# Optimization experiments

Measured on AMD Instinct MI355X. Metric: run time of the kernel, lower is better.

The kernel has to match this reference:

```python
import jax, jax.numpy as jnp
import numpy as np

N = 100000
K = 27  # 3^3 kernel offsets for dimension=3
EPS = 1e-6


def layer_norm(x, gamma, beta):
    mu = jnp.mean(x, axis=-1, keepdims=True)
    var = jnp.mean(jnp.square(x - mu), axis=-1, keepdims=True)
    return (x - mu) * jax.lax.rsqrt(var + EPS) * gamma + beta


def sparse_conv3(x, idx, mask, W):
    # gather-GEMM-scatter form of Minkowski sparse conv:
    # x: [N, Cin], idx/mask: [N, K], W: [K, Cin, Cout]
    xg = jnp.where(mask[..., None], x[idx], 0.0)  # [N, K, Cin]
    return jnp.einsum('nkc,kcd->nd', xg, W)


def setup_inputs() -> dict:
    key = jax.random.key(0)
    ks = jax.random.split(key, 6)
    x = jax.random.normal(ks[0], (N, 32), dtype=jnp.float32)
    neighbor_idx = jax.random.randint(ks[1], (N, K), 0, N, dtype=jnp.int32)
    neighbor_mask = jax.random.randint(ks[2], (N, K), 0, 2) > 0
    W_conv = jax.random.normal(ks[3], (32, 32), dtype=jnp.float32) * 0.1
    W1 = jax.random.normal(ks[4], (K, 32, 128), dtype=jnp.float32) * 0.05
    W2 = jax.random.normal(ks[5], (K, 128, 32), dtype=jnp.float32) * 0.05
    return {
        'x': x,
        'neighbor_idx': neighbor_idx,
        'neighbor_mask': neighbor_mask,
        'W_conv': W_conv,
        'gamma0': jnp.ones((32,), jnp.float32),
        'beta0': jnp.zeros((32,), jnp.float32),
        'W1': W1,
        'gamma1': jnp.ones((128,), jnp.float32),
        'beta1': jnp.zeros((128,), jnp.float32),
        'W2': W2,
        'gamma2': jnp.ones((32,), jnp.float32),
        'beta2': jnp.zeros((32,), jnp.float32),
    }


def reference(x, neighbor_idx, neighbor_mask, W_conv, gamma0, beta0,
              W1, gamma1, beta1, W2, gamma2, beta2):
    gelu = lambda t: jax.nn.gelu(t, approximate=False)  # torch default (erf)
    residual = x
    out = x @ W_conv                      # kernel_size=1 conv == dense matmul
    out = gelu(layer_norm(out, gamma0, beta0))
    out = sparse_conv3(out, neighbor_idx, neighbor_mask, W1)
    out = gelu(layer_norm(out, gamma1, beta1))
    out = sparse_conv3(out, neighbor_idx, neighbor_mask, W2)
    out = layer_norm(out, gamma2, beta2)
    out = out + residual
    return gelu(out)
```

## Files before the change

### kernel.cpp

```cpp
#include <hip/hip_runtime.h>
#include <hip/hip_bf16.h>
#include <math.h>

#define NPTS 100000
#define KOFF 27

typedef __attribute__((ext_vector_type(8))) __bf16 bf16x8;
typedef __attribute__((ext_vector_type(4))) float f32x4;

__device__ __forceinline__ unsigned short f2bf(float f) {
    unsigned int u = __float_as_uint(f);
    u += 0x7fffu + ((u >> 16) & 1u);
    return (unsigned short)(u >> 16);
}

__device__ __forceinline__ float gelu_erf(float v) {
    return 0.5f * v * (1.0f + erff(v * 0.70710678118654752f));
}

__global__ __launch_bounds__(256)
void repack_kernel(const float* __restrict__ W1, const float* __restrict__ W2,
                   const void* __restrict__ maskp,
                   unsigned short* __restrict__ W1p,
                   unsigned short* __restrict__ W2p,
                   int* __restrict__ flagp) {
    int o = blockIdx.x * 256 + threadIdx.x;
    if (o == 0) {
        const unsigned int* mw = (const unsigned int*)maskp;
        int f = 0;
        for (int i = 0; i < 64; ++i) f |= (mw[i] > 1u) ? 1 : 0;
        *flagp = f;
    }
    if (o < KOFF * 32 * 128) {
        int j = o & 7, lane = (o >> 3) & 63;
        int quad = lane >> 4, nn = lane & 15;
        int ct1 = (o >> 9) & 7, k1 = o >> 12;
        int kk1 = quad * 8 + j;
        W1p[o] = f2bf(W1[(k1 * 32 + kk1) * 128 + (ct1 * 16 + nn)]);
        int ct2 = (o >> 9) & 1, kc2 = (o >> 10) & 3, k2 = o >> 12;
        int kk2 = kc2 * 32 + quad * 8 + j;
        W2p[o] = f2bf(W2[(k2 * 128 + kk2) * 32 + (ct2 * 16 + nn)]);
    }
}

__global__ __launch_bounds__(256)
void conv1_ln_gelu(const float* __restrict__ x, const float* __restrict__ Wc,
                   const float* __restrict__ g0, const float* __restrict__ b0,
                   unsigned short* __restrict__ out0) {
    __shared__ float xs[256];
    __shared__ float wc[1024];
    int t = threadIdx.x;
    int nb = blockIdx.x * 8;
    xs[t] = x[nb * 32 + t];
    for (int i = t; i < 1024; i += 256) wc[i] = Wc[i];
    __syncthreads();
    int r = t >> 5, d = t & 31;
    const float* xr = &xs[r * 32];
    float v = 0.f;
#pragma unroll
    for (int c = 0; c < 32; ++c) v = fmaf(xr[c], wc[c * 32 + d], v);
    float s = v, s2 = v * v;
#pragma unroll
    for (int m = 16; m >= 1; m >>= 1) {
        s  += __shfl_xor(s,  m, 32);
        s2 += __shfl_xor(s2, m, 32);
    }
    float mu  = s * (1.f / 32.f);
    float var = s2 * (1.f / 32.f) - mu * mu;
    float y = (v - mu) * rsqrtf(var + 1e-6f) * g0[d] + b0[d];
    out0[nb * 32 + t] = f2bf(gelu_erf(y));
}

__device__ __forceinline__ void stage_gidx64(int* s_gidx, const int* nidx,
                                             const void* maskp, int mflag,
                                             int nb, int t) {
    int cnt = (NPTS - nb < 64 ? NPTS - nb : 64) * KOFF;
    for (int i = t; i < 64 * KOFF; i += 64) {
        int g = -1;
        if (i < cnt) {
            int gi = nidx[nb * KOFF + i];
            int m = mflag ? (int)((const unsigned char*)maskp)[nb * KOFF + i]
                          : ((const int*)maskp)[nb * KOFF + i];
            g = m ? gi : -1;
        }
        s_gidx[i] = g;
    }
}

__global__ __launch_bounds__(64, 2)
void conv_k1(const int* __restrict__ nidx, const void* __restrict__ maskp,
             const int* __restrict__ flagp,
             const unsigned short* __restrict__ out0,
             const unsigned short* __restrict__ W1p,
             const float* __restrict__ g1, const float* __restrict__ b1,
             unsigned short* __restrict__ out1) {
    __shared__ int s_gidx[64 * KOFF];

    int t = threadIdx.x;
    int nb = blockIdx.x * 64;
    int mflag = *flagp;
    stage_gidx64(s_gidx, nidx, maskp, mflag, nb, t);
    __syncthreads();

    int lane = t & 63;
    int mrow = lane & 15, quad = lane >> 4;
    const unsigned short* a_base = out0 + quad * 8;
    const int* gp0 = &s_gidx[(0 * 16 + mrow) * KOFF];
    const int* gp1 = &s_gidx[(1 * 16 + mrow) * KOFF];
    const int* gp2 = &s_gidx[(2 * 16 + mrow) * KOFF];
    const int* gp3 = &s_gidx[(3 * 16 + mrow) * KOFF];

    f32x4 acc[4][8] = {};
    bf16x8 a[2][4], b[2][8];

    {
        const unsigned short* wb = W1p + (lane << 3);
#pragma unroll
        for (int ct = 0; ct < 8; ++ct)
            b[0][ct] = *reinterpret_cast<const bf16x8*>(wb + ((ct * 64) << 3));
        int g0 = gp0[0], g1i = gp1[0], g2 = gp2[0], g3 = gp3[0];
        a[0][0] = bf16x8{}; if (g0  >= 0) a[0][0] = *reinterpret_cast<const bf16x8*>(a_base + g0  * 32);
        a[0][1] = bf16x8{}; if (g1i >= 0) a[0][1] = *reinterpret_cast<const bf16x8*>(a_base + g1i * 32);
        a[0][2] = bf16x8{}; if (g2  >= 0) a[0][2] = *reinterpret_cast<const bf16x8*>(a_base + g2  * 32);
        a[0][3] = bf16x8{}; if (g3  >= 0) a[0][3] = *reinterpret_cast<const bf16x8*>(a_base + g3  * 32);
    }

#pragma unroll
    for (int k = 0; k < KOFF; ++k) {
        int cur = k & 1, nxt = cur ^ 1;
        if (k + 1 < KOFF) {
            const unsigned short* wb = W1p + ((((k + 1) * 8) * 64 + lane) << 3);
#pragma unroll
            for (int ct = 0; ct < 8; ++ct)
                b[nxt][ct] = *reinterpret_cast<const bf16x8*>(wb + ((ct * 64) << 3));
            int g0 = gp0[k + 1], g1i = gp1[k + 1], g2 = gp2[k + 1], g3 = gp3[k + 1];
            a[nxt][0] = bf16x8{}; if (g0  >= 0) a[nxt][0] = *reinterpret_cast<const bf16x8*>(a_base + g0  * 32);
            a[nxt][1] = bf16x8{}; if (g1i >= 0) a[nxt][1] = *reinterpret_cast<const bf16x8*>(a_base + g1i * 32);
            a[nxt][2] = bf16x8{}; if (g2  >= 0) a[nxt][2] = *reinterpret_cast<const bf16x8*>(a_base + g2  * 32);
            a[nxt][3] = bf16x8{}; if (g3  >= 0) a[nxt][3] = *reinterpret_cast<const bf16x8*>(a_base + g3  * 32);
        }
#pragma unroll
        for (int rt = 0; rt < 4; ++rt)
#pragma unroll
            for (int ct = 0; ct < 8; ++ct)
                acc[rt][ct] = __builtin_amdgcn_mfma_f32_16x16x32_bf16(a[cur][rt], b[cur][ct], acc[rt][ct], 0, 0, 0);
    }

    float gv[8], bv[8];
#pragma unroll
    for (int ct = 0; ct < 8; ++ct) {
        gv[ct] = g1[ct * 16 + mrow];
        bv[ct] = b1[ct * 16 + mrow];
    }
#pragma unroll
    for (int rt = 0; rt < 4; ++rt) {
        int n_base = nb + rt * 16 + quad * 4;
#pragma unroll
        for (int r = 0; r < 4; ++r) {
            float s = 0.f, s2 = 0.f;
#pragma unroll
            for (int ct = 0; ct < 8; ++ct) { float v = acc[rt][ct][r]; s += v; s2 += v * v; }
#pragma unroll
            for (int m = 1; m <= 8; m <<= 1) {
                s  += __shfl_xor(s,  m, 16);
                s2 += __shfl_xor(s2, m, 16);
            }
            float mu = s * (1.f / 128.f);
            float rs = rsqrtf(s2 * (1.f / 128.f) - mu * mu + 1e-6f);
            int n = n_base + r;
            if (n < NPTS) {
#pragma unroll
                for (int ct = 0; ct < 8; ++ct) {
                    float y = (acc[rt][ct][r] - mu) * rs * gv[ct] + bv[ct];
                    out1[n * 128 + ct * 16 + mrow] = f2bf(gelu_erf(y));
                }
            }
        }
    }
}

__global__ __launch_bounds__(64, 2)
void gemm_tmp(const unsigned short* __restrict__ out1,
              const unsigned short* __restrict__ W2p,
              unsigned short* __restrict__ tmp) {
    int t = threadIdx.x;
    int nb = blockIdx.x * 64;
    int mrow = t & 15, quad = t >> 4;

    bf16x8 a[4][4];
#pragma unroll
    for (int rt = 0; rt < 4; ++rt) {
        int n = nb + rt * 16 + mrow;
        bool ok = (n < NPTS);
#pragma unroll
        for (int kc = 0; kc < 4; ++kc) {
            a[rt][kc] = bf16x8{};
            if (ok)
                a[rt][kc] = *reinterpret_cast<const bf16x8*>(out1 + (size_t)n * 128 + kc * 32 + quad * 8);
        }
    }
    bf16x8 b[2][8];
    {
        const unsigned short* wb = W2p + (t << 3);
#pragma unroll
        for (int f = 0; f < 8; ++f)
            b[0][f] = *reinterpret_cast<const bf16x8*>(wb + ((f * 64) << 3));
    }

#pragma unroll
    for (int k = 0; k < KOFF; ++k) {
        int cur = k & 1, nxt = cur ^ 1;
        if (k + 1 < KOFF) {
            const unsigned short* wb = W2p + ((((k + 1) * 8) * 64 + t) << 3);
#pragma unroll
            for (int f = 0; f < 8; ++f)
                b[nxt][f] = *reinterpret_cast<const bf16x8*>(wb + ((f * 64) << 3));
        }
        f32x4 acc[4][2] = {};
#pragma unroll
        for (int rt = 0; rt < 4; ++rt)
#pragma unroll
            for (int kc = 0; kc < 4; ++kc) {
                acc[rt][0] = __builtin_amdgcn_mfma_f32_16x16x32_bf16(a[rt][kc], b[cur][kc * 2 + 0], acc[rt][0], 0, 0, 0);
                acc[rt][1] = __builtin_amdgcn_mfma_f32_16x16x32_bf16(a[rt][kc], b[cur][kc * 2 + 1], acc[rt][1], 0, 0, 0);
            }
        unsigned short* tk = tmp + (size_t)k * NPTS * 32;
#pragma unroll
        for (int rt = 0; rt < 4; ++rt) {
            int n0 = nb + rt * 16 + quad * 4;
#pragma unroll
            for (int r = 0; r < 4; ++r) {
                int n = n0 + r;
                if (n < NPTS) {
#pragma unroll
                    for (int ct = 0; ct < 2; ++ct)
                        tk[(size_t)n * 32 + ct * 16 + mrow] = f2bf(acc[rt][ct][r]);
                }
            }
        }
    }
}

__global__ __launch_bounds__(256)
void gather_sum(const int* __restrict__ nidx, const void* __restrict__ maskp,
                const int* __restrict__ flagp,
                const unsigned short* __restrict__ tmp,
                const float* __restrict__ g2, const float* __restrict__ b2,
                const float* __restrict__ x, float* __restrict__ outp) {
    __shared__ int s_gidx[64 * KOFF];
    int t = threadIdx.x;
    int nb = blockIdx.x * 64;
    int mflag = *flagp;
    int cnt = (NPTS - nb < 64 ? NPTS - nb : 64) * KOFF;
    for (int i = t; i < 64 * KOFF; i += 256) {
        int g = -1;
        if (i < cnt) {
            int gi = nidx[nb * KOFF + i];
            int m = mflag ? (int)((const unsigned char*)maskp)[nb * KOFF + i]
                          : ((const int*)maskp)[nb * KOFF + i];
            g = m ? gi : -1;
        }
        s_gidx[i] = g;
    }
    __syncthreads();

    int rl = t >> 2, q = t & 3;
    const int* gp = &s_gidx[rl * KOFF];
    const unsigned short* tq = tmp + q * 8;

    float acc[8] = {};
    uint4 ring[3];
#pragma unroll
    for (int d = 0; d < 3; ++d) {
        int g = gp[d];
        ring[d] = uint4{0u, 0u, 0u, 0u};
        if (g >= 0)
            ring[d] = *reinterpret_cast<const uint4*>(tq + ((size_t)d * NPTS + g) * 32);
    }
#pragma unroll
    for (int k = 0; k < KOFF; ++k) {
        uint4 v = ring[k % 3];
        if (k + 3 < KOFF) {
            int g = gp[k + 3];
            ring[k % 3] = uint4{0u, 0u, 0u, 0u};
            if (g >= 0)
                ring[k % 3] = *reinterpret_cast<const uint4*>(tq + ((size_t)(k + 3) * NPTS + g) * 32);
        }
        unsigned int w0 = v.x, w1 = v.y, w2 = v.z, w3 = v.w;
        acc[0] += __uint_as_float(w0 << 16);
        acc[1] += __uint_as_float(w0 & 0xffff0000u);
        acc[2] += __uint_as_float(w1 << 16);
        acc[3] += __uint_as_float(w1 & 0xffff0000u);
        acc[4] += __uint_as_float(w2 << 16);
        acc[5] += __uint_as_float(w2 & 0xffff0000u);
        acc[6] += __uint_as_float(w3 << 16);
        acc[7] += __uint_as_float(w3 & 0xffff0000u);
    }

    float s = 0.f, s2 = 0.f;
#pragma unroll
    for (int j = 0; j < 8; ++j) { s += acc[j]; s2 += acc[j] * acc[j]; }
    s += __shfl_xor(s, 1); s2 += __shfl_xor(s2, 1);
    s += __shfl_xor(s, 2); s2 += __shfl_xor(s2, 2);
    float mu = s * (1.f / 32.f);
    float rs = rsqrtf(s2 * (1.f / 32.f) - mu * mu + 1e-6f);

    int n = nb + rl;
    if (n < NPTS) {
        float o[8];
#pragma unroll
        for (int j = 0; j < 8; ++j) {
            int c = q * 8 + j;
            float y = (acc[j] - mu) * rs * g2[c] + b2[c] + x[n * 32 + c];
            o[j] = gelu_erf(y);
        }
        *reinterpret_cast<float4*>(outp + n * 32 + q * 8)     = make_float4(o[0], o[1], o[2], o[3]);
        *reinterpret_cast<float4*>(outp + n * 32 + q * 8 + 4) = make_float4(o[4], o[5], o[6], o[7]);
    }
}

__global__ __launch_bounds__(64, 2)
void conv_k2_fb(const int* __restrict__ nidx, const void* __restrict__ maskp,
                const int* __restrict__ flagp,
                const unsigned short* __restrict__ out1,
                const unsigned short* __restrict__ W2p,
                const float* __restrict__ g2, const float* __restrict__ b2,
                const float* __restrict__ x, float* __restrict__ outp) {
    __shared__ int s_gidx[64 * KOFF];

    int t = threadIdx.x;
    int nb = blockIdx.x * 64;
    int mflag = *flagp;
    stage_gidx64(s_gidx, nidx, maskp, mflag, nb, t);
    __syncthreads();

    int lane = t & 63;
    int mrow = lane & 15, quad = lane >> 4;
    const unsigned short* a_base = out1 + quad * 8;
    const int* gp0 = &s_gidx[(0 * 16 + mrow) * KOFF];
    const int* gp1 = &s_gidx[(1 * 16 + mrow) * KOFF];
    const int* gp2 = &s_gidx[(2 * 16 + mrow) * KOFF];
    const int* gp3 = &s_gidx[(3 * 16 + mrow) * KOFF];

    f32x4 acc[4][2] = {};
    bf16x8 a[2][4][4], b[2][8];

    {
        const unsigned short* wb = W2p + (lane << 3);
#pragma unroll
        for (int f = 0; f < 8; ++f)
            b[0][f] = *reinterpret_cast<const bf16x8*>(wb + ((f * 64) << 3));
        int gg[4] = { gp0[0], gp1[0], gp2[0], gp3[0] };
#pragma unroll
        for (int rt = 0; rt < 4; ++rt) {
#pragma unroll
            for (int kc = 0; kc < 4; ++kc) a[0][rt][kc] = bf16x8{};
            if (gg[rt] >= 0) {
#pragma unroll
                for (int kc = 0; kc < 4; ++kc)
                    a[0][rt][kc] = *reinterpret_cast<const bf16x8*>(a_base + (size_t)gg[rt] * 128 + kc * 32);
            }
        }
    }

#pragma unroll
    for (int k = 0; k < KOFF; ++k) {
        int cur = k & 1, nxt = cur ^ 1;
        if (k + 1 < KOFF) {
            const unsigned short* wb = W2p + ((((k + 1) * 8) * 64 + lane) << 3);
#pragma unroll
            for (int f = 0; f < 8; ++f)
                b[nxt][f] = *reinterpret_cast<const bf16x8*>(wb + ((f * 64) << 3));
            int gg[4] = { gp0[k + 1], gp1[k + 1], gp2[k + 1], gp3[k + 1] };
#pragma unroll
            for (int rt = 0; rt < 4; ++rt) {
#pragma unroll
                for (int kc = 0; kc < 4; ++kc) a[nxt][rt][kc] = bf16x8{};
                if (gg[rt] >= 0) {
#pragma unroll
                    for (int kc = 0; kc < 4; ++kc)
                        a[nxt][rt][kc] = *reinterpret_cast<const bf16x8*>(a_base + (size_t)gg[rt] * 128 + kc * 32);
                }
            }
        }
#pragma unroll
        for (int rt = 0; rt < 4; ++rt)
#pragma unroll
            for (int kc = 0; kc < 4; ++kc) {
                acc[rt][0] = __builtin_amdgcn_mfma_f32_16x16x32_bf16(a[cur][rt][kc], b[cur][kc * 2 + 0], acc[rt][0], 0, 0, 0);
                acc[rt][1] = __builtin_amdgcn_mfma_f32_16x16x32_bf16(a[cur][rt][kc], b[cur][kc * 2 + 1], acc[rt][1], 0, 0, 0);
            }
    }

    float gv0 = g2[mrow], gv1 = g2[mrow + 16];
    float bv0 = b2[mrow], bv1 = b2[mrow + 16];
#pragma unroll
    for (int rt = 0; rt < 4; ++rt) {
        int n_base = nb + rt * 16 + quad * 4;
#pragma unroll
        for (int r = 0; r < 4; ++r) {
            float v0 = acc[rt][0][r], v1 = acc[rt][1][r];
            float s = v0 + v1, s2 = v0 * v0 + v1 * v1;
#pragma unroll
            for (int m = 1; m <= 8; m <<= 1) {
                s  += __shfl_xor(s,  m, 16);
                s2 += __shfl_xor(s2, m, 16);
            }
            float mu = s * (1.f / 32.f);
            float rs = rsqrtf(s2 * (1.f / 32.f) - mu * mu + 1e-6f);
            int n = n_base + r;
            if (n < NPTS) {
                float y0 = (v0 - mu) * rs * gv0 + bv0 + x[n * 32 + mrow];
                float y1 = (v1 - mu) * rs * gv1 + bv1 + x[n * 32 + mrow + 16];
                outp[n * 32 + mrow]      = gelu_erf(y0);
                outp[n * 32 + mrow + 16] = gelu_erf(y1);
            }
        }
    }
}

extern "C" void kernel_launch(void* const* d_in, const int* in_sizes, int n_in,
                              void* d_out, int out_size, void* d_ws, size_t ws_size,
                              hipStream_t stream) {
    const float* x    = (const float*)d_in[0];
    const int*   nidx = (const int*)d_in[1];
    const void*  maskp = d_in[2];
    const float* Wc = (const float*)d_in[3];
    const float* g0 = (const float*)d_in[4];
    const float* b0 = (const float*)d_in[5];
    const float* W1 = (const float*)d_in[6];
    const float* g1 = (const float*)d_in[7];
    const float* b1 = (const float*)d_in[8];
    const float* W2 = (const float*)d_in[9];
    const float* g2 = (const float*)d_in[10];
    const float* b2 = (const float*)d_in[11];

    char* ws = (char*)d_ws;
    unsigned short* out0 = (unsigned short*)ws;
    unsigned short* out1 = (unsigned short*)(ws + 6400000);
    unsigned short* W1p  = (unsigned short*)(ws + 32000000);
    unsigned short* W2p  = (unsigned short*)(ws + 32221184);
    int* flagp           = (int*)(ws + 32442368);
    unsigned short* tmp  = (unsigned short*)(ws + 32442432);
    const size_t NEED_TMP = 32442432UL + (size_t)KOFF * NPTS * 32 * 2;

    repack_kernel<<<432, 256, 0, stream>>>(W1, W2, maskp, W1p, W2p, flagp);
    conv1_ln_gelu<<<NPTS / 8, 256, 0, stream>>>(x, Wc, g0, b0, out0);
    conv_k1<<<(NPTS + 63) / 64, 64, 0, stream>>>(nidx, maskp, flagp, out0, W1p, g1, b1, out1);
    if (ws_size >= NEED_TMP) {
        gemm_tmp<<<(NPTS + 63) / 64, 64, 0, stream>>>(out1, W2p, tmp);
        gather_sum<<<(NPTS + 63) / 64, 256, 0, stream>>>(nidx, maskp, flagp, tmp, g2, b2, x, (float*)d_out);
    } else {
        conv_k2_fb<<<(NPTS + 63) / 64, 64, 0, stream>>>(nidx, maskp, flagp, out1, W2p, g2, b2, x, (float*)d_out);
    }
}
```

Measured before the change: 277.8 us.

## Shrink conv_k1 tile with triple-buffered prefetch; pack tmp stores via interleaved W2

conv_k1 now processes 32 rows per block instead of 64 and uses a three-deep register prefetch of gathered rows and weights. This frees registers and launches more blocks for better latency hiding, at the cost of reloading weights more often. A second W2 repack interleaves output columns so gemm_tmp can write two bf16 values as one 32-bit store. gather_sum's prefetch ring is also deepened from 3 to 4.

Result: faster. 269.7 us (-2.9%).

```diff
diff --git a/kernel.cpp b/kernel.cpp
--- a/kernel.cpp
+++ b/kernel.cpp
@@ -23,6 +23,7 @@
                    const void* __restrict__ maskp,
                    unsigned short* __restrict__ W1p,
                    unsigned short* __restrict__ W2p,
+                   unsigned short* __restrict__ W2q,
                    int* __restrict__ flagp) {
     int o = blockIdx.x * 256 + threadIdx.x;
     if (o == 0) {
@@ -40,6 +41,7 @@
         int ct2 = (o >> 9) & 1, kc2 = (o >> 10) & 3, k2 = o >> 12;
         int kk2 = kc2 * 32 + quad * 8 + j;
         W2p[o] = f2bf(W2[(k2 * 128 + kk2) * 32 + (ct2 * 16 + nn)]);
+        W2q[o] = f2bf(W2[(k2 * 128 + kk2) * 32 + (2 * nn + ct2)]);
     }
 }
 
@@ -94,12 +96,19 @@
              const unsigned short* __restrict__ W1p,
              const float* __restrict__ g1, const float* __restrict__ b1,
              unsigned short* __restrict__ out1) {
-    __shared__ int s_gidx[64 * KOFF];
+    __shared__ int s_gidx[32 * KOFF];
 
     int t = threadIdx.x;
-    int nb = blockIdx.x * 64;
+    int nb = blockIdx.x * 32;
     int mflag = *flagp;
-    stage_gidx64(s_gidx, nidx, maskp, mflag, nb, t);
+    {
+        for (int i = t; i < 32 * KOFF; i += 64) {
+            int gi = nidx[nb * KOFF + i];
+            int m = mflag ? (int)((const unsigned char*)maskp)[nb * KOFF + i]
+                          : ((const int*)maskp)[nb * KOFF + i];
+            s_gidx[i] = m ? gi : -1;
+        }
+    }
     __syncthreads();
 
     int lane = t & 63;
@@ -107,43 +116,38 @@
     const unsigned short* a_base = out0 + quad * 8;
     const int* gp0 = &s_gidx[(0 * 16 + mrow) * KOFF];
     const int* gp1 = &s_gidx[(1 * 16 + mrow) * KOFF];
-    const int* gp2 = &s_gidx[(2 * 16 + mrow) * KOFF];
-    const int* gp3 = &s_gidx[(3 * 16 + mrow) * KOFF];
-
-    f32x4 acc[4][8] = {};
-    bf16x8 a[2][4], b[2][8];
-
-    {
-        const unsigned short* wb = W1p + (lane << 3);
+
+    f32x4 acc[2][8] = {};
+    bf16x8 a[3][2], b[3][8];
+
+#pragma unroll
+    for (int d = 0; d < 2; ++d) {
+        const unsigned short* wb = W1p + (((d * 8) * 64 + lane) << 3);
 #pragma unroll
         for (int ct = 0; ct < 8; ++ct)
-            b[0][ct] = *reinterpret_cast<const bf16x8*>(wb + ((ct * 64) << 3));
-        int g0 = gp0[0], g1i = gp1[0], g2 = gp2[0], g3 = gp3[0];
-        a[0][0] = bf16x8{}; if (g0  >= 0) a[0][0] = *reinterpret_cast<const bf16x8*>(a_base + g0  * 32);
-        a[0][1] = bf16x8{}; if (g1i >= 0) a[0][1] = *reinterpret_cast<const bf16x8*>(a_base + g1i * 32);
-        a[0][2] = bf16x8{}; if (g2  >= 0) a[0][2] = *reinterpret_cast<const bf16x8*>(a_base + g2  * 32);
-        a[0][3] = bf16x8{}; if (g3  >= 0) a[0][3] = *reinterpret_cast<const bf16x8*>(a_base + g3  * 32);
+            b[d][ct] = *reinterpret_cast<const bf16x8*>(wb + ((ct * 64) << 3));
+        int g0 = gp0[d], g1i = gp1[d];
+        a[d][0] = bf16x8{}; if (g0  >= 0) a[d][0] = *reinterpret_cast<const bf16x8*>(a_base + g0  * 32);
+        a[d][1] = bf16x8{}; if (g1i >= 0) a[d][1] = *reinterpret_cast<const bf16x8*>(a_base + g1i * 32);
     }
 
 #pragma unroll
     for (int k = 0; k < KOFF; ++k) {
-        int cur = k & 1, nxt = cur ^ 1;
-        if (k + 1 < KOFF) {
-            const unsigned short* wb = W1p + ((((k + 1) * 8) * 64 + lane) << 3);
+        if (k + 2 < KOFF) {
+            int s = (k + 2) % 3;
+            const unsigned short* wb = W1p + ((((k + 2) * 8) * 64 + lane) << 3);
 #pragma unroll
             for (int ct = 0; ct < 8; ++ct)
-                b[nxt][ct] = *reinterpret_cast<const bf16x8*>(wb + ((ct * 64) << 3));
-            int g0 = gp0[k + 1], g1i = gp1[k + 1], g2 = gp2[k + 1], g3 = gp3[k + 1];
-            a[nxt][0] = bf16x8{}; if (g0  >= 0) a[nxt][0] = *reinterpret_cast<const bf16x8*>(a_base + g0  * 32);
-            a[nxt][1] = bf16x8{}; if (g1i >= 0) a[nxt][1] = *reinterpret_cast<const bf16x8*>(a_base + g1i * 32);
-            a[nxt][2] = bf16x8{}; if (g2  >= 0) a[nxt][2] = *reinterpret_cast<const bf16x8*>(a_base + g2  * 32);
-            a[nxt][3] = bf16x8{}; if (g3  >= 0) a[nxt][3] = *reinterpret_cast<const bf16x8*>(a_base + g3  * 32);
-        }
-#pragma unroll
-        for (int rt = 0; rt < 4; ++rt)
+                b[s][ct] = *reinterpret_cast<const bf16x8*>(wb + ((ct * 64) << 3));
+            int g0 = gp0[k + 2], g1i = gp1[k + 2];
+            a[s][0] = bf16x8{}; if (g0  >= 0) a[s][0] = *reinterpret_cast<const bf16x8*>(a_base + g0  * 32);
+            a[s][1] = bf16x8{}; if (g1i >= 0) a[s][1] = *reinterpret_cast<const bf16x8*>(a_base + g1i * 32);
+        }
+#pragma unroll
+        for (int rt = 0; rt < 2; ++rt)
 #pragma unroll
             for (int ct = 0; ct < 8; ++ct)
-                acc[rt][ct] = __builtin_amdgcn_mfma_f32_16x16x32_bf16(a[cur][rt], b[cur][ct], acc[rt][ct], 0, 0, 0);
+                acc[rt][ct] = __builtin_amdgcn_mfma_f32_16x16x32_bf16(a[k % 3][rt], b[k % 3][ct], acc[rt][ct], 0, 0, 0);
     }
 
     float gv[8], bv[8];
@@ -153,7 +157,7 @@
         bv[ct] = b1[ct * 16 + mrow];
     }
 #pragma unroll
-    for (int rt = 0; rt < 4; ++rt) {
+    for (int rt = 0; rt < 2; ++rt) {
         int n_base = nb + rt * 16 + quad * 4;
 #pragma unroll
         for (int r = 0; r < 4; ++r) {
@@ -168,12 +172,10 @@
             float mu = s * (1.f / 128.f);
             float rs = rsqrtf(s2 * (1.f / 128.f) - mu * mu + 1e-6f);
             int n = n_base + r;
-            if (n < NPTS) {
-#pragma unroll
-                for (int ct = 0; ct < 8; ++ct) {
-                    float y = (acc[rt][ct][r] - mu) * rs * gv[ct] + bv[ct];
-                    out1[n * 128 + ct * 16 + mrow] = f2bf(gelu_erf(y));
-                }
+#pragma unroll
+            for (int ct = 0; ct < 8; ++ct) {
+                float y = (acc[rt][ct][r] - mu) * rs * gv[ct] + bv[ct];
+                out1[n * 128 + ct * 16 + mrow] = f2bf(gelu_erf(y));
             }
         }
     }
@@ -181,7 +183,7 @@
 
 __global__ __launch_bounds__(64, 2)
 void gemm_tmp(const unsigned short* __restrict__ out1,
-              const unsigned short* __restrict__ W2p,
+              const unsigned short* __restrict__ W2q,
               unsigned short* __restrict__ tmp) {
     int t = threadIdx.x;
     int nb = blockIdx.x * 64;
@@ -201,7 +203,7 @@
     }
     bf16x8 b[2][8];
     {
-        const unsigned short* wb = W2p + (t << 3);
+        const unsigned short* wb = W2q + (t << 3);
 #pragma unroll
         for (int f = 0; f < 8; ++f)
             b[0][f] = *reinterpret_cast<const bf16x8*>(wb + ((f * 64) << 3));
@@ -211,7 +213,7 @@
     for (int k = 0; k < KOFF; ++k) {
         int cur = k & 1, nxt = cur ^ 1;
         if (k + 1 < KOFF) {
-            const unsigned short* wb = W2p + ((((k + 1) * 8) * 64 + t) << 3);
+            const unsigned short* wb = W2q + ((((k + 1) * 8) * 64 + t) << 3);
 #pragma unroll
             for (int f = 0; f < 8; ++f)
                 b[nxt][f] = *reinterpret_cast<const bf16x8*>(wb + ((f * 64) << 3));
@@ -224,7 +226,7 @@
                 acc[rt][0] = __builtin_amdgcn_mfma_f32_16x16x32_bf16(a[rt][kc], b[cur][kc * 2 + 0], acc[rt][0], 0, 0, 0);
                 acc[rt][1] = __builtin_amdgcn_mfma_f32_16x16x32_bf16(a[rt][kc], b[cur][kc * 2 + 1], acc[rt][1], 0, 0, 0);
             }
-        unsigned short* tk = tmp + (size_t)k * NPTS * 32;
+        unsigned int* tk32 = (unsigned int*)(tmp + (size_t)k * NPTS * 32);
 #pragma unroll
         for (int rt = 0; rt < 4; ++rt) {
             int n0 = nb + rt * 16 + quad * 4;
@@ -232,9 +234,9 @@
             for (int r = 0; r < 4; ++r) {
                 int n = n0 + r;
                 if (n < NPTS) {
-#pragma unroll
-                    for (int ct = 0; ct < 2; ++ct)
-                        tk[(size_t)n * 32 + ct * 16 + mrow] = f2bf(acc[rt][ct][r]);
+                    unsigned int pk = (unsigned int)f2bf(acc[rt][0][r])
+                                    | ((unsigned int)f2bf(acc[rt][1][r]) << 16);
+                    tk32[(size_t)n * 16 + mrow] = pk;
                 }
             }
         }
@@ -269,9 +271,9 @@
     const unsigned short* tq = tmp + q * 8;
 
     float acc[8] = {};
-    uint4 ring[3];
-#pragma unroll
-    for (int d = 0; d < 3; ++d) {
+    uint4 ring[4];
+#pragma unroll
+    for (int d = 0; d < 4; ++d) {
         int g = gp[d];
         ring[d] = uint4{0u, 0u, 0u, 0u};
         if (g >= 0)
@@ -279,12 +281,12 @@
     }
 #pragma unroll
     for (int k = 0; k < KOFF; ++k) {
-        uint4 v = ring[k % 3];
-        if (k + 3 < KOFF) {
-            int g = gp[k + 3];
-            ring[k % 3] = uint4{0u, 0u, 0u, 0u};
+        uint4 v = ring[k & 3];
+        if (k + 4 < KOFF) {
+            int g = gp[k + 4];
+            ring[k & 3] = uint4{0u, 0u, 0u, 0u};
             if (g >= 0)
-                ring[k % 3] = *reinterpret_cast<const uint4*>(tq + ((size_t)(k + 3) * NPTS + g) * 32);
+                ring[k & 3] = *reinterpret_cast<const uint4*>(tq + ((size_t)(k + 4) * NPTS + g) * 32);
         }
         unsigned int w0 = v.x, w1 = v.y, w2 = v.z, w3 = v.w;
         acc[0] += __uint_as_float(w0 << 16);
@@ -440,15 +442,16 @@
     unsigned short* out1 = (unsigned short*)(ws + 6400000);
     unsigned short* W1p  = (unsigned short*)(ws + 32000000);
     unsigned short* W2p  = (unsigned short*)(ws + 32221184);
-    int* flagp           = (int*)(ws + 32442368);
-    unsigned short* tmp  = (unsigned short*)(ws + 32442432);
-    const size_t NEED_TMP = 32442432UL + (size_t)KOFF * NPTS * 32 * 2;
-
-    repack_kernel<<<432, 256, 0, stream>>>(W1, W2, maskp, W1p, W2p, flagp);
+    unsigned short* W2q  = (unsigned short*)(ws + 32442368);
+    int* flagp           = (int*)(ws + 32663552);
+    unsigned short* tmp  = (unsigned short*)(ws + 32663616);
+    const size_t NEED_TMP = 32663616UL + (size_t)KOFF * NPTS * 32 * 2;
+
+    repack_kernel<<<432, 256, 0, stream>>>(W1, W2, maskp, W1p, W2p, W2q, flagp);
     conv1_ln_gelu<<<NPTS / 8, 256, 0, stream>>>(x, Wc, g0, b0, out0);
-    conv_k1<<<(NPTS + 63) / 64, 64, 0, stream>>>(nidx, maskp, flagp, out0, W1p, g1, b1, out1);
+    conv_k1<<<NPTS / 32, 64, 0, stream>>>(nidx, maskp, flagp, out0, W1p, g1, b1, out1);
     if (ws_size >= NEED_TMP) {
-        gemm_tmp<<<(NPTS + 63) / 64, 64, 0, stream>>>(out1, W2p, tmp);
+        gemm_tmp<<<(NPTS + 63) / 64, 64, 0, stream>>>(out1, W2q, tmp);
         gather_sum<<<(NPTS + 63) / 64, 256, 0, stream>>>(nidx, maskp, flagp, tmp, g2, b2, x, (float*)d_out);
     } else {
         conv_k2_fb<<<(NPTS + 63) / 64, 64, 0, stream>>>(nidx, maskp, flagp, out1, W2p, g2, b2, x, (float*)d_out);
```
